# Kernel optimization log

Measured on AMD Instinct MI355X. Metric: run time of the kernel, lower is better.

## Reference

```python
import jax, jax.numpy as jnp
import numpy as np

N_AGENTS = 2048   # total valid agents across the batch
R_CAND = 128      # ROI candidates per agent (uniform spans)
NUM_MODS = 6
T = 30            # num_preds
B = 16            # scenes in batch
REG_COEF = 1.0
IOU_THR = 0.5


def setup_inputs() -> dict:
    key = jax.random.key(0)
    ks = jax.random.split(key, 6)
    roi_feat = jax.random.normal(ks[0], (N_AGENTS * R_CAND, 5), jnp.float32) * 0.5
    anchor_pose = jax.random.normal(ks[1], (N_AGENTS * R_CAND, 4), jnp.float32) * 3.0
    ctrs = jax.random.normal(ks[2], (N_AGENTS, 2), jnp.float32) * 3.0
    feats = jax.random.normal(ks[3], (N_AGENTS, 20, 3), jnp.float32) * 0.3
    gt_preds = jax.random.normal(ks[4], (N_AGENTS, T, 2), jnp.float32) * 3.0
    has_preds = jnp.ones((N_AGENTS, T), dtype=bool)
    num_atgs_per_batch = jnp.full((B,), N_AGENTS // B, dtype=jnp.int32)
    return dict(roi_feat=roi_feat, anchor_pose=anchor_pose, ctrs=ctrs,
                feats=feats, gt_preds=gt_preds, has_preds=has_preds,
                num_atgs_per_batch=num_atgs_per_batch)


def _iou_matrix(boxes):
    # boxes: [R, 4] in x1y1x2y2
    area = (boxes[:, 2] - boxes[:, 0]) * (boxes[:, 3] - boxes[:, 1])
    lt = jnp.maximum(boxes[:, None, :2], boxes[None, :, :2])
    rb = jnp.minimum(boxes[:, None, 2:], boxes[None, :, 2:])
    wh = jnp.clip(rb - lt, 0.0)
    inter = wh[..., 0] * wh[..., 1]
    return inter / (area[:, None] + area[None, :] - inter)


def _nms_keep(boxes, scores):
    # Greedy NMS (torchvision semantics): score-descending, suppress IoU > thr.
    R = boxes.shape[0]
    order = jnp.argsort(-scores)
    iou = _iou_matrix(boxes[order])
    idx = jnp.arange(R)

    def step(keep, i):
        sup = jnp.any(keep & (idx < i) & (iou[:, i] > IOU_THR))
        return keep.at[i].set(~sup), None

    keep_sorted, _ = jax.lax.scan(step, jnp.ones(R, dtype=bool), idx)
    return jnp.zeros(R, dtype=bool).at[order].set(keep_sorted)


def _select_agent(anchor, pred, gt_last):
    # anchor [R,4], pred [R,5], gt_last [2]
    logics = pred[:, 0]
    goals = anchor + pred[:, 1:]
    boxes = jnp.concatenate([goals[:, :2] - 0.25, goals[:, :2] + 0.25], -1)
    keep = _nms_keep(boxes, logics)
    # fallback: if fewer than num_mods survive, keep all (idxs = arange)
    keep = jnp.where(keep.sum() >= NUM_MODS, keep, jnp.ones_like(keep))
    # torch: sqrt(d**2).sum(-1) == L1 distance to gt end point
    dist = jnp.abs(goals[:, :2] - gt_last[None, :]).sum(-1)
    dist = jnp.where(keep, dist, jnp.inf)
    top = jnp.argsort(dist)[:NUM_MODS]
    return logics[top], goals[top]  # [6], [6,4]


def reference(roi_feat, anchor_pose, ctrs, feats, gt_preds, has_preds, num_atgs_per_batch):
    anchors = anchor_pose.reshape(N_AGENTS, R_CAND, 4)
    preds = roi_feat.reshape(N_AGENTS, R_CAND, 5)
    logics, sel = jax.vmap(_select_agent)(anchors, preds, gt_preds[:, -1])  # [N,6],[N,6,4]

    # agent pose = [ctr_x, ctr_y, dir_x, dir_y] from last history step
    ap = jnp.concatenate([ctrs, feats[:, -1, :2]], -1)[:, None, :]  # [N,1,4]

    a1 = (2 * sel[..., 0] * ap[..., 2] + 2 * ap[..., 0] * ap[..., 2]) / (2.0 + ap[..., 2] - sel[..., 2])
    a0 = sel[..., 0] - ap[..., 0] - a1
    a2 = jnp.broadcast_to(ap[..., 0], a0.shape)
    b1 = (2 * sel[..., 1] * ap[..., 3] + 2 * ap[..., 1] * ap[..., 3]) / (2.0 + ap[..., 3] - sel[..., 3])
    b0 = sel[..., 1] - ap[..., 1] - b1
    b2 = jnp.broadcast_to(ap[..., 1], b0.shape)

    s = jnp.arange(T, dtype=jnp.float32) / (T - 1)  # [30]
    x = a0[..., None] * s ** 2 + a1[..., None] * s + a2[..., None]  # [N,6,30]
    y = b0[..., None] * s ** 2 + b1[..., None] * s + b2[..., None]
    pred_trajs = jnp.stack([x, y], -1)  # [N,6,30,2]

    hasf = has_preds.astype(jnp.float32)
    last = hasf + 0.1 * jnp.arange(T, dtype=jnp.float32) / float(T)
    max_last = last.max(1)
    last_idcs = last.argmax(1)
    mask = max_last > 1.0  # [N]

    rows = jnp.arange(N_AGENTS)
    end_pred = pred_trajs[rows, :, last_idcs]        # [N,6,2]
    end_gt = gt_preds[rows, last_idcs]               # [N,2]
    dist = jnp.sqrt(((end_pred - end_gt[:, None, :]) ** 2).sum(-1))  # [N,6]
    min_idcs = dist.argmin(-1)

    # cls: BCE-with-logits vs one-hot best mode, sum over masked agents
    logic_gt = jax.nn.one_hot(min_idcs, NUM_MODS, dtype=jnp.float32)
    bce = jnp.maximum(logics, 0.0) - logics * logic_gt + jnp.log1p(jnp.exp(-jnp.abs(logics)))
    cls_loss = (bce * mask[:, None]).sum()
    num_cls = mask.sum()

    # reg: SmoothL1 (sum) on best mode, masked agents & valid timesteps
    best = pred_trajs[rows, min_idcs]  # [N,30,2]
    diff = best - gt_preds
    ad = jnp.abs(diff)
    sl1 = jnp.where(ad < 1.0, 0.5 * diff * diff, ad - 0.5)
    w = (mask[:, None] & has_preds).astype(jnp.float32)  # [N,30]
    reg_loss = REG_COEF * (sl1 * w[..., None]).sum()
    num_reg = w.sum()

    # traj_to_eval: faithful to original temp = [0] + num_atgs_per_batch[:-1]
    temp = jnp.concatenate([jnp.zeros((1,), num_atgs_per_batch.dtype), num_atgs_per_batch[:-1]])
    traj_eval = pred_trajs[temp]  # [B,6,30,2]

    return cls_loss, reg_loss, traj_eval, num_cls, num_reg
```

## Files before the change

kernel.cpp:

```cpp
#include <hip/hip_runtime.h>
#include <math.h>
#include <stdint.h>

#define N_AGENTS 2048
#define R_CAND   128
#define NUM_MODS 6
#define T_STEPS  30
#define B_BATCH  16


__global__ __launch_bounds__(256) void agent_kernel(
    const float* __restrict__ roi,
    const float* __restrict__ anchor,
    const float* __restrict__ ctrs,
    const float* __restrict__ feats,
    const float* __restrict__ gt,
    const int* __restrict__ has,
    const int* __restrict__ natgs,
    float* __restrict__ out,
    float* __restrict__ part)
{
    const int a   = blockIdx.x;
    const int tid = threadIdx.x;

    __shared__ float4   s_goal[R_CAND];
    __shared__ float    s_logic[R_CAND];
    __shared__ float2   s_pos[R_CAND];
    __shared__ float    s_d[R_CAND];
    __shared__ __align__(16) uint32_t s_col[R_CAND][4];
    __shared__ float    s_gtrow[T_STEPS * 2];
    __shared__ int      s_has[T_STEPS];
    __shared__ float    s_coef[NUM_MODS][6];
    __shared__ float    s_traj[NUM_MODS][T_STEPS][2];

    float gx = 0.0f, gy = 0.0f;
    if (tid < R_CAND) {
        const float* rp  = roi + (size_t)(a * R_CAND + tid) * 5;
        const float4 anc = *reinterpret_cast<const float4*>(anchor + (size_t)(a * R_CAND + tid) * 4);
        const float lg = rp[0];
        gx = anc.x + rp[1];
        gy = anc.y + rp[2];
        s_logic[tid] = lg;
        s_goal[tid]  = make_float4(gx, gy, anc.z + rp[3], anc.w + rp[4]);
        s_pos[tid]   = make_float2(gx, gy);
        *reinterpret_cast<uint4*>(&s_col[tid][0]) = make_uint4(0u, 0u, 0u, 0u);
    } else if (tid < 128 + 60) {
        s_gtrow[tid - 128] = gt[(size_t)a * T_STEPS * 2 + (tid - 128)];
    } else if (tid >= 192 && tid < 192 + T_STEPS) {
        s_has[tid - 192] = has[(size_t)a * T_STEPS + (tid - 192)];
    }
    __syncthreads();

    {
        const int c = tid & 127, hf = tid >> 7;
        if (hf == 0) s_d[c] = fabsf(gx - s_gtrow[(T_STEPS - 1) * 2]) +
                              fabsf(gy - s_gtrow[(T_STEPS - 1) * 2 + 1]);
        const float2 pt = s_pos[c];
        const int dlo = hf ? 33 : 1;
        const int dhi = hf ? ((c < 64) ? 64 : 63) : 32;
        for (int d = dlo; d <= dhi; ++d) {
            const int p = (c + d) & (R_CAND - 1);
            const float2 pp = s_pos[p];
            const float wx = 0.5f - fabsf(pt.x - pp.x);
            const float wy = 0.5f - fabsf(pt.y - pp.y);
            if (wx > 0.0f && wx * wy > (1.0f / 6.0f)) {
                const float lgc = s_logic[c], lgp = s_logic[p];
                const int p_wins = (lgp > lgc) || (lgp == lgc && p < c);
                const int sup  = p_wins ? c : p;
                const int by   = p_wins ? p : c;
                atomicOr(&s_col[sup][by >> 5], 1u << (by & 31));
            }
        }
    }
    __syncthreads();

    float my_slog = 0.0f; int my_win = 0;
    if (tid < 64) {
        const uint64_t cA0 = (uint64_t)s_col[tid][0]      | ((uint64_t)s_col[tid][1]      << 32);
        const uint64_t cA1 = (uint64_t)s_col[tid][2]      | ((uint64_t)s_col[tid][3]      << 32);
        const uint64_t cB0 = (uint64_t)s_col[tid + 64][0] | ((uint64_t)s_col[tid + 64][1] << 32);
        const uint64_t cB1 = (uint64_t)s_col[tid + 64][2] | ((uint64_t)s_col[tid + 64][3] << 32);
        uint64_t k0 = ~0ull, k1 = ~0ull;
        for (int it = 0; it < 200; ++it) {
            const int slo = (((cA0 & k0) | (cA1 & k1)) != 0);
            const int shi = (((cB0 & k0) | (cB1 & k1)) != 0);
            const uint64_t n0 = ~__ballot(slo);
            const uint64_t n1 = ~__ballot(shi);
            if (n0 == k0 && n1 == k1) break;
            k0 = n0; k1 = n1;
        }
        const int kfall = (__popcll(k0) + __popcll(k1)) < NUM_MODS;
        float d_lo = (kfall | (int)((k0 >> tid) & 1)) ? s_d[tid]      : INFINITY;
        float d_hi = (kfall | (int)((k1 >> tid) & 1)) ? s_d[tid + 64] : INFINITY;
        int   i_lo = tid, i_hi = tid + 64;
        for (int m = 0; m < NUM_MODS; ++m) {
            float bd; int bi;
            if (d_lo < d_hi || (d_lo == d_hi && i_lo < i_hi)) { bd = d_lo; bi = i_lo; }
            else                                               { bd = d_hi; bi = i_hi; }
            for (int off = 32; off >= 1; off >>= 1) {
                const float od = __shfl_down(bd, (unsigned)off, 64);
                const int   oi = __shfl_down(bi, (unsigned)off, 64);
                if (od < bd || (od == bd && oi < bi)) { bd = od; bi = oi; }
            }
            bi = __shfl(bi, 0, 64);
            if (tid == m) my_win = bi;
            if (i_lo == bi) d_lo = INFINITY;
            if (i_hi == bi) d_hi = INFINITY;
        }
        if (tid < NUM_MODS) {
            const float ap0 = ctrs[(size_t)a * 2 + 0];
            const float ap1 = ctrs[(size_t)a * 2 + 1];
            const float ap2 = feats[((size_t)a * 20 + 19) * 3 + 0];
            const float ap3 = feats[((size_t)a * 20 + 19) * 3 + 1];
            const float4 g = s_goal[my_win];
            my_slog = s_logic[my_win];
            const float a1c = (2.f * g.x * ap2 + 2.f * ap0 * ap2) / (2.f + ap2 - g.z);
            const float a0c = g.x - ap0 - a1c;
            const float b1c = (2.f * g.y * ap3 + 2.f * ap1 * ap3) / (2.f + ap3 - g.w);
            const float b0c = g.y - ap1 - b1c;
            s_coef[tid][0] = a0c; s_coef[tid][1] = a1c; s_coef[tid][2] = ap0;
            s_coef[tid][3] = b0c; s_coef[tid][4] = b1c; s_coef[tid][5] = ap1;
        }
    }
    __syncthreads();

    if (tid < NUM_MODS * T_STEPS) {
        const int m = tid / T_STEPS, t = tid % T_STEPS;
        const float s1 = (float)t / (float)(T_STEPS - 1);
        const float s2 = s1 * s1;
        s_traj[m][t][0] = s_coef[m][0] * s2 + s_coef[m][1] * s1 + s_coef[m][2];
        s_traj[m][t][1] = s_coef[m][3] * s2 + s_coef[m][4] * s1 + s_coef[m][5];
    }
    __syncthreads();

    if (tid < 64) {
        float bv = -1e30f; int bt = tid;
        if (tid < T_STEPS) bv = (s_has[tid] ? 1.0f : 0.0f) + (0.1f * (float)tid) / (float)T_STEPS;
        for (int off = 16; off >= 1; off >>= 1) {
            const float ov = __shfl_down(bv, (unsigned)off, 32);
            const int   ot = __shfl_down(bt, (unsigned)off, 32);
            if (ov > bv || (ov == bv && ot < bt)) { bv = ov; bt = ot; }
        }
        const int   lt   = __shfl(bt, 0, 64);
        const float bmax = __shfl(bv, 0, 64);
        const int   mask = bmax > 1.0f;
        const float egx = s_gtrow[lt * 2 + 0], egy = s_gtrow[lt * 2 + 1];
        float md = 1e30f; int mm = tid;
        if (tid < NUM_MODS) {
            const float dx = s_traj[tid][lt][0] - egx;
            const float dy = s_traj[tid][lt][1] - egy;
            md = sqrtf(dx * dx + dy * dy);
        }
        for (int off = 4; off >= 1; off >>= 1) {
            const float ov = __shfl_down(md, (unsigned)off, 8);
            const int   om = __shfl_down(mm, (unsigned)off, 8);
            if (ov < md || (ov == md && om < mm)) { md = ov; mm = om; }
        }
        const int mi = __shfl(mm, 0, 64);
        float cv = 0.0f;
        if (tid < NUM_MODS) {
            const float l = my_slog;
            const float g = (tid == mi) ? 1.0f : 0.0f;
            cv = fmaxf(l, 0.0f) - l * g + log1pf(expf(-fabsf(l)));
        }
        cv += __shfl_xor(cv, 4, 8); cv += __shfl_xor(cv, 2, 8); cv += __shfl_xor(cv, 1, 8);
        float rv = 0.0f;
        if (tid < 2 * T_STEPS) {
            const int t = tid >> 1, c = tid & 1;
            if (mask && s_has[t]) {
                const float diff = s_traj[mi][t][c] - s_gtrow[t * 2 + c];
                const float ad = fabsf(diff);
                rv = (ad < 1.0f) ? 0.5f * diff * diff : (ad - 0.5f);
            }
        }
        for (int off = 32; off >= 1; off >>= 1) rv += __shfl_xor(rv, (unsigned)off, 64);
        const int hv = (tid < T_STEPS) ? s_has[tid] : 0;
        const int nh = __popcll(__ballot(hv != 0));
        if (tid == 0) {
            *reinterpret_cast<float4*>(&part[(size_t)a * 4]) =
                make_float4(mask ? cv : 0.0f, rv, mask ? 1.0f : 0.0f, mask ? (float)nh : 0.0f);
        }
    } else if (tid < 128) {
        const float* tp = &s_traj[0][0][0];
        const int p = tid - 64;
        for (int b = 0; b < B_BATCH; ++b) {
            const int target = (b == 0) ? 0 : natgs[b - 1];
            if (target == a) {
                for (int q = p; q < NUM_MODS * T_STEPS * 2; q += 64)
                    out[2 + (size_t)b * NUM_MODS * T_STEPS * 2 + q] = tp[q];
            }
        }
    }
}

__global__ __launch_bounds__(256) void reduce_kernel(
    const float* __restrict__ part, float* __restrict__ out)
{
    __shared__ double s0[256], s1[256], s2[256], s3[256];
    const int tid = threadIdx.x;
    double c = 0, r = 0, n = 0, w = 0;
    for (int a = tid; a < N_AGENTS; a += 256) {
        c += (double)part[(size_t)a * 4 + 0];
        r += (double)part[(size_t)a * 4 + 1];
        n += (double)part[(size_t)a * 4 + 2];
        w += (double)part[(size_t)a * 4 + 3];
    }
    s0[tid] = c; s1[tid] = r; s2[tid] = n; s3[tid] = w;
    __syncthreads();
    for (int off = 128; off >= 1; off >>= 1) {
        if (tid < off) {
            s0[tid] += s0[tid + off]; s1[tid] += s1[tid + off];
            s2[tid] += s2[tid + off]; s3[tid] += s3[tid + off];
        }
        __syncthreads();
    }
    if (tid == 0) {
        out[0]    = (float)s0[0];
        out[1]    = (float)s1[0];
        out[5762] = (float)s2[0];
        out[5763] = (float)s3[0];
    }
}

extern "C" void kernel_launch(void* const* d_in, const int* in_sizes, int n_in,
                              void* d_out, int out_size, void* d_ws, size_t ws_size,
                              hipStream_t stream) {
    const float*   roi    = (const float*)d_in[0];
    const float*   anchor = (const float*)d_in[1];
    const float*   ctrs   = (const float*)d_in[2];
    const float*   feats  = (const float*)d_in[3];
    const float*   gt     = (const float*)d_in[4];
    const int*     has    = (const int*)d_in[5];
    const int*     natgs  = (const int*)d_in[6];
    float* out  = (float*)d_out;
    float* part = (float*)d_ws;

    agent_kernel<<<N_AGENTS, 256, 0, stream>>>(roi, anchor, ctrs, feats, gt, has, natgs, out, part);
    reduce_kernel<<<1, 256, 0, stream>>>(part, out);
}
```

Measured before the change: 22.76 us.

## Drop trajectory smem stage, unroll pairwise NMS loop, shrink final reduction to one wave

Removes the s_traj shared-memory buffer and its barrier, recomputing the quadratic trajectory points from the coefficients wherever they are needed. The pairwise overlap loop is unrolled to two candidates per iteration, using a padded s_pos entry to avoid wraparound, and the thread's own position and logit are kept in registers. The reduce kernel becomes a single 64-lane wave that loads float4 values and reduces with shuffles instead of a shared-memory tree with many barriers. The cost is some redundant arithmetic in exchange for fewer barriers and less shared memory.

```diff
diff --git a/kernel.cpp b/kernel.cpp
--- a/kernel.cpp
+++ b/kernel.cpp
@@ -25,24 +25,24 @@
 
     __shared__ float4   s_goal[R_CAND];
     __shared__ float    s_logic[R_CAND];
-    __shared__ float2   s_pos[R_CAND];
+    __shared__ float2   s_pos[R_CAND + 1];
     __shared__ float    s_d[R_CAND];
     __shared__ __align__(16) uint32_t s_col[R_CAND][4];
     __shared__ float    s_gtrow[T_STEPS * 2];
     __shared__ int      s_has[T_STEPS];
     __shared__ float    s_coef[NUM_MODS][6];
-    __shared__ float    s_traj[NUM_MODS][T_STEPS][2];
-
-    float gx = 0.0f, gy = 0.0f;
+
+    float lg = 0.0f, gx = 0.0f, gy = 0.0f;
     if (tid < R_CAND) {
         const float* rp  = roi + (size_t)(a * R_CAND + tid) * 5;
         const float4 anc = *reinterpret_cast<const float4*>(anchor + (size_t)(a * R_CAND + tid) * 4);
-        const float lg = rp[0];
+        lg = rp[0];
         gx = anc.x + rp[1];
         gy = anc.y + rp[2];
         s_logic[tid] = lg;
         s_goal[tid]  = make_float4(gx, gy, anc.z + rp[3], anc.w + rp[4]);
         s_pos[tid]   = make_float2(gx, gy);
+        if (tid == 0) s_pos[R_CAND] = make_float2(gx, gy);
         *reinterpret_cast<uint4*>(&s_col[tid][0]) = make_uint4(0u, 0u, 0u, 0u);
     } else if (tid < 128 + 60) {
         s_gtrow[tid - 128] = gt[(size_t)a * T_STEPS * 2 + (tid - 128)];
@@ -53,22 +53,39 @@
 
     {
         const int c = tid & 127, hf = tid >> 7;
-        if (hf == 0) s_d[c] = fabsf(gx - s_gtrow[(T_STEPS - 1) * 2]) +
-                              fabsf(gy - s_gtrow[(T_STEPS - 1) * 2 + 1]);
-        const float2 pt = s_pos[c];
-        const int dlo = hf ? 33 : 1;
-        const int dhi = hf ? ((c < 64) ? 64 : 63) : 32;
-        for (int d = dlo; d <= dhi; ++d) {
-            const int p = (c + d) & (R_CAND - 1);
-            const float2 pp = s_pos[p];
-            const float wx = 0.5f - fabsf(pt.x - pp.x);
-            const float wy = 0.5f - fabsf(pt.y - pp.y);
-            if (wx > 0.0f && wx * wy > (1.0f / 6.0f)) {
-                const float lgc = s_logic[c], lgp = s_logic[p];
-                const int p_wins = (lgp > lgc) || (lgp == lgc && p < c);
-                const int sup  = p_wins ? c : p;
-                const int by   = p_wins ? p : c;
-                atomicOr(&s_col[sup][by >> 5], 1u << (by & 31));
+        const float2 pt = (tid < 128) ? make_float2(gx, gy) : s_pos[c];
+        if (hf == 0) s_d[c] = fabsf(pt.x - s_gtrow[(T_STEPS - 1) * 2]) +
+                              fabsf(pt.y - s_gtrow[(T_STEPS - 1) * 2 + 1]);
+        const float lgc = (tid < 128) ? lg : s_logic[c];
+        const int d0 = hf ? 33 : 1;
+        #pragma unroll 4
+        for (int i = 0; i < 16; ++i) {
+            const int dd = d0 + 2 * i;
+            const int p0 = (c + dd) & (R_CAND - 1);
+            const float2 pa = s_pos[p0];
+            const float2 pb = s_pos[p0 + 1];
+            {
+                const float wx = 0.5f - fabsf(pt.x - pa.x);
+                const float wy = 0.5f - fabsf(pt.y - pa.y);
+                if (wx > 0.0f && wx * wy > (1.0f / 6.0f)) {
+                    const float lgp = s_logic[p0];
+                    const int p_wins = (lgp > lgc) || (lgp == lgc && p0 < c);
+                    const int sup = p_wins ? c : p0;
+                    const int by  = p_wins ? p0 : c;
+                    atomicOr(&s_col[sup][by >> 5], 1u << (by & 31));
+                }
+            }
+            if (dd != 63 || c < 64) {
+                const int p1 = (p0 + 1) & (R_CAND - 1);
+                const float wx = 0.5f - fabsf(pt.x - pb.x);
+                const float wy = 0.5f - fabsf(pt.y - pb.y);
+                if (wx > 0.0f && wx * wy > (1.0f / 6.0f)) {
+                    const float lgp = s_logic[p1];
+                    const int p_wins = (lgp > lgc) || (lgp == lgc && p1 < c);
+                    const int sup = p_wins ? c : p1;
+                    const int by  = p_wins ? p1 : c;
+                    atomicOr(&s_col[sup][by >> 5], 1u << (by & 31));
+                }
             }
         }
     }
@@ -124,15 +141,6 @@
     }
     __syncthreads();
 
-    if (tid < NUM_MODS * T_STEPS) {
-        const int m = tid / T_STEPS, t = tid % T_STEPS;
-        const float s1 = (float)t / (float)(T_STEPS - 1);
-        const float s2 = s1 * s1;
-        s_traj[m][t][0] = s_coef[m][0] * s2 + s_coef[m][1] * s1 + s_coef[m][2];
-        s_traj[m][t][1] = s_coef[m][3] * s2 + s_coef[m][4] * s1 + s_coef[m][5];
-    }
-    __syncthreads();
-
     if (tid < 64) {
         float bv = -1e30f; int bt = tid;
         if (tid < T_STEPS) bv = (s_has[tid] ? 1.0f : 0.0f) + (0.1f * (float)tid) / (float)T_STEPS;
@@ -147,8 +155,11 @@
         const float egx = s_gtrow[lt * 2 + 0], egy = s_gtrow[lt * 2 + 1];
         float md = 1e30f; int mm = tid;
         if (tid < NUM_MODS) {
-            const float dx = s_traj[tid][lt][0] - egx;
-            const float dy = s_traj[tid][lt][1] - egy;
+            const float s1 = (float)lt / (float)(T_STEPS - 1);
+            const float s2 = s1 * s1;
+            const float tx = s_coef[tid][0] * s2 + s_coef[tid][1] * s1 + s_coef[tid][2];
+            const float ty = s_coef[tid][3] * s2 + s_coef[tid][4] * s1 + s_coef[tid][5];
+            const float dx = tx - egx, dy = ty - egy;
             md = sqrtf(dx * dx + dy * dy);
         }
         for (int off = 4; off >= 1; off >>= 1) {
@@ -168,7 +179,10 @@
         if (tid < 2 * T_STEPS) {
             const int t = tid >> 1, c = tid & 1;
             if (mask && s_has[t]) {
-                const float diff = s_traj[mi][t][c] - s_gtrow[t * 2 + c];
+                const float s1 = (float)t / (float)(T_STEPS - 1);
+                const float s2 = s1 * s1;
+                const float tv = s_coef[mi][3 * c] * s2 + s_coef[mi][3 * c + 1] * s1 + s_coef[mi][3 * c + 2];
+                const float diff = tv - s_gtrow[t * 2 + c];
                 const float ad = fabsf(diff);
                 rv = (ad < 1.0f) ? 0.5f * diff * diff : (ad - 0.5f);
             }
@@ -181,44 +195,43 @@
                 make_float4(mask ? cv : 0.0f, rv, mask ? 1.0f : 0.0f, mask ? (float)nh : 0.0f);
         }
     } else if (tid < 128) {
-        const float* tp = &s_traj[0][0][0];
         const int p = tid - 64;
         for (int b = 0; b < B_BATCH; ++b) {
             const int target = (b == 0) ? 0 : natgs[b - 1];
             if (target == a) {
-                for (int q = p; q < NUM_MODS * T_STEPS * 2; q += 64)
-                    out[2 + (size_t)b * NUM_MODS * T_STEPS * 2 + q] = tp[q];
+                for (int q = p; q < NUM_MODS * T_STEPS * 2; q += 64) {
+                    const int m = q / 60, rem = q % 60;
+                    const int t = rem >> 1, c = rem & 1;
+                    const float s1 = (float)t / (float)(T_STEPS - 1);
+                    const float s2 = s1 * s1;
+                    const float tv = s_coef[m][3 * c] * s2 + s_coef[m][3 * c + 1] * s1 + s_coef[m][3 * c + 2];
+                    out[2 + (size_t)b * NUM_MODS * T_STEPS * 2 + q] = tv;
+                }
             }
         }
     }
 }
 
-__global__ __launch_bounds__(256) void reduce_kernel(
-    const float* __restrict__ part, float* __restrict__ out)
+__global__ __launch_bounds__(64) void reduce_kernel(
+    const float4* __restrict__ part4, float* __restrict__ out)
 {
-    __shared__ double s0[256], s1[256], s2[256], s3[256];
-    const int tid = threadIdx.x;
+    const int lane = threadIdx.x;
     double c = 0, r = 0, n = 0, w = 0;
-    for (int a = tid; a < N_AGENTS; a += 256) {
-        c += (double)part[(size_t)a * 4 + 0];
-        r += (double)part[(size_t)a * 4 + 1];
-        n += (double)part[(size_t)a * 4 + 2];
-        w += (double)part[(size_t)a * 4 + 3];
-    }
-    s0[tid] = c; s1[tid] = r; s2[tid] = n; s3[tid] = w;
-    __syncthreads();
-    for (int off = 128; off >= 1; off >>= 1) {
-        if (tid < off) {
-            s0[tid] += s0[tid + off]; s1[tid] += s1[tid + off];
-            s2[tid] += s2[tid + off]; s3[tid] += s3[tid + off];
-        }
-        __syncthreads();
-    }
-    if (tid == 0) {
-        out[0]    = (float)s0[0];
-        out[1]    = (float)s1[0];
-        out[5762] = (float)s2[0];
-        out[5763] = (float)s3[0];
+    for (int a = lane; a < N_AGENTS; a += 64) {
+        const float4 v = part4[a];
+        c += (double)v.x; r += (double)v.y; n += (double)v.z; w += (double)v.w;
+    }
+    for (int off = 32; off >= 1; off >>= 1) {
+        c += __shfl_down(c, (unsigned)off, 64);
+        r += __shfl_down(r, (unsigned)off, 64);
+        n += __shfl_down(n, (unsigned)off, 64);
+        w += __shfl_down(w, (unsigned)off, 64);
+    }
+    if (lane == 0) {
+        out[0]    = (float)c;
+        out[1]    = (float)r;
+        out[5762] = (float)n;
+        out[5763] = (float)w;
     }
 }
 
@@ -236,5 +249,5 @@
     float* part = (float*)d_ws;
 
     agent_kernel<<<N_AGENTS, 256, 0, stream>>>(roi, anchor, ctrs, feats, gt, has, natgs, out, part);
-    reduce_kernel<<<1, 256, 0, stream>>>(part, out);
+    reduce_kernel<<<1, 64, 0, stream>>>((const float4*)part, out);
 }
```

New measurement: 31.51 us. 38.4% more time.
